# Performance work log

Measured on AMD Instinct MI355X. Metric: run time of the kernel, lower is better.

Reference implementation:

```python
import jax, jax.numpy as jnp
import numpy as np

H = 64   # LSTM hidden size
NL = 8   # LSTM layers
B, T = 2048, 64


def setup_inputs() -> dict:
    key = jax.random.key(0)
    ks = jax.random.split(key, 18)
    r = lambda i, shape, s=0.1: jax.random.normal(ks[i], shape, dtype=jnp.float32) * s
    return {
        "x": r(0, (B, T, 2), 1.0),
        "w1": r(1, (16, 2)), "b1": r(2, (16,)),
        "w2": r(3, (16, 16)), "b2": r(4, (16,)),
        "w_ih0": r(5, (4 * H, 16)), "w_hh0": r(6, (4 * H, H)),
        "b_ih0": r(7, (4 * H,)), "b_hh0": r(8, (4 * H,)),
        "w_ih": r(9, (NL - 1, 4 * H, H)), "w_hh": r(10, (NL - 1, 4 * H, H)),
        "b_ih": r(11, (NL - 1, 4 * H)), "b_hh": r(12, (NL - 1, 4 * H)),
        "wo1": r(13, (32, H)), "bo1": r(14, (32,)),
        "wo2": r(15, (4, 32)), "bo2": r(16, (4,)),
    }


def _lstm_layer(x, w_ih, w_hh, b):
    # x: [B, T, I]; torch gate order: i, f, g, o
    bsz = x.shape[0]
    xg = jnp.einsum('bti,gi->btg', x, w_ih) + b  # [B, T, 4H] precomputed input gates

    def step(carry, xg_t):
        h, c = carry
        gates = xg_t + h @ w_hh.T
        i, f, g, o = jnp.split(gates, 4, axis=-1)
        i = jax.nn.sigmoid(i); f = jax.nn.sigmoid(f)
        g = jnp.tanh(g); o = jax.nn.sigmoid(o)
        c = f * c + i * g
        h = o * jnp.tanh(c)
        return (h, c), h

    h0 = jnp.zeros((bsz, H), x.dtype)
    _, hs = jax.lax.scan(step, (h0, h0), jnp.swapaxes(xg, 0, 1))  # [T, B, H]
    return jnp.swapaxes(hs, 0, 1)


def reference(x, w1, b1, w2, b2, w_ih0, w_hh0, b_ih0, b_hh0,
              w_ih, w_hh, b_ih, b_hh, wo1, bo1, wo2, bo2):
    # action-input MLP: 2 -> 16 -> relu -> 16
    h = jax.nn.relu(x @ w1.T + b1) @ w2.T + b2
    # 8-layer LSTM, hidden 64
    h = _lstm_layer(h, w_ih0, w_hh0, b_ih0 + b_hh0)
    for l in range(NL - 1):
        h = _lstm_layer(h, w_ih[l], w_hh[l], b_ih[l] + b_hh[l])
    # output MLP: 64 -> 32 -> relu -> 4
    return jax.nn.relu(h @ wo1.T + bo1) @ wo2.T + bo2
```

## Files before the change

kernel.cpp:

```cpp
#include <hip/hip_runtime.h>


#define BATCH 2048
#define TT 64
#define HH 64
#define LDP 136

typedef short bf16x8 __attribute__((ext_vector_type(8)));
typedef float f32x4 __attribute__((ext_vector_type(4)));

__device__ __forceinline__ float sigmoid_fast(float x) {
    return __builtin_amdgcn_rcpf(1.f + __expf(-x));
}
__device__ __forceinline__ float tanh_fast(float x) {
    float e = __expf(-2.f * x);
    e = fminf(e, 1e30f);
    return (1.f - e) * __builtin_amdgcn_rcpf(1.f + e);
}
__device__ __forceinline__ void split2(float x, unsigned short& hi, unsigned short& lo) {
    const unsigned u = __float_as_uint(x);
    hi = (unsigned short)(u >> 16);
    const float r = x - __uint_as_float(u & 0xFFFF0000u);
    lo = (unsigned short)(__float_as_uint(r) >> 16);
}
__device__ __forceinline__ void wg_wait(int* c, int v) {
    while (__hip_atomic_load(c, __ATOMIC_ACQUIRE, __HIP_MEMORY_SCOPE_WORKGROUP) < v)
        __builtin_amdgcn_s_sleep(1);
}
__device__ __forceinline__ void wg_bump(int* c, int lane) {
    if (lane == 0)
        __hip_atomic_fetch_add(c, 1, __ATOMIC_RELEASE, __HIP_MEMORY_SCOPE_WORKGROUP);
}

__global__ __launch_bounds__(256)
void mlp_in_kernel(const float* __restrict__ x,
                   const float* __restrict__ w1, const float* __restrict__ b1,
                   const float* __restrict__ w2, const float* __restrict__ b2,
                   float* __restrict__ out) {
    const int gid = blockIdx.x * 256 + threadIdx.x;
    const float x0 = x[gid * 2 + 0];
    const float x1 = x[gid * 2 + 1];
    float hid[16];
#pragma unroll
    for (int j = 0; j < 16; ++j) {
        float v = fmaf(x1, w1[j * 2 + 1], fmaf(x0, w1[j * 2 + 0], b1[j]));
        hid[j] = fmaxf(0.f, v);
    }
    float o[16];
#pragma unroll
    for (int oo = 0; oo < 16; ++oo) {
        float acc = b2[oo];
#pragma unroll
        for (int j = 0; j < 16; ++j) acc = fmaf(hid[j], w2[oo * 16 + j], acc);
        o[oo] = acc;
    }
    float4* op = (float4*)(out + gid * 16);
#pragma unroll
    for (int q = 0; q < 4; ++q) {
        float4 v;
        v.x = o[q * 4 + 0]; v.y = o[q * 4 + 1]; v.z = o[q * 4 + 2]; v.w = o[q * 4 + 3];
        op[q] = v;
    }
}

template <int IA, int IPADA>
__global__ __launch_bounds__(512, 2)
void lstm_pair(const float* __restrict__ xmlp,
               unsigned* __restrict__ P,
               float* __restrict__ houtf,
               const int last,
               const float* __restrict__ wihA, const float* __restrict__ whhA,
               const float* __restrict__ biA, const float* __restrict__ bhA,
               const float* __restrict__ wihB, const float* __restrict__ whhB,
               const float* __restrict__ biB, const float* __restrict__ bhB) {
    constexpr int KTA = (IPADA + 64) / 32;
    __shared__ unsigned short pAh[2][16 * LDP], pAl[2][16 * LDP];
    __shared__ unsigned short pBh[2][16 * LDP], pBl[2][16 * LDP];
    __shared__ int cA, cB;

    const int tid = threadIdx.x;
    const int wv = tid >> 6, lane = tid & 63, l16 = lane & 15, quad = lane >> 4;
    const int grp = wv >> 2;
    const int wg = wv & 3;
    const int base = blockIdx.x * 8;
    const bool lo32 = (lane < 32);
    const int bpi = (lane & 31) << 2;

    if (tid == 0) { cA = 0; cB = 0; }
    for (int e = tid; e < 2 * 16 * LDP; e += 512) {
        (&pAh[0][0])[e] = 0; (&pAl[0][0])[e] = 0;
        (&pBh[0][0])[e] = 0; (&pBl[0][0])[e] = 0;
    }

    const int I    = grp ? 64 : IA;
    const int IPAD = grp ? 64 : IPADA;
    const int KT   = grp ? 4  : KTA;
    const float* wih = grp ? wihB : wihA;
    const float* whh = grp ? whhB : whhA;
    const float* bi  = grp ? biB  : biA;
    const float* bh  = grp ? bhB  : bhA;

    const int jg = 16 * wg + l16;
    bf16x8 bhi[4][4], blo[4][4];
    float bsum[4];
#pragma unroll
    for (int gt = 0; gt < 4; ++gt) {
        const int n = gt * 64 + jg;
        bsum[gt] = bi[n] + bh[n];
#pragma unroll
        for (int kt = 0; kt < 4; ++kt) {
            bf16x8 vh = {0, 0, 0, 0, 0, 0, 0, 0};
            bf16x8 vl = {0, 0, 0, 0, 0, 0, 0, 0};
            if (kt < KT) {
#pragma unroll
                for (int j = 0; j < 8; ++j) {
                    const int k = kt * 32 + quad * 8 + j;
                    float w = 0.f;
                    if (k < I) w = wih[n * I + k];
                    else if (k >= IPAD) w = whh[n * 64 + (k - IPAD)];
                    unsigned short h_, l_;
                    split2(w, h_, l_);
                    vh[j] = (short)h_;
                    vl[j] = (short)l_;
                }
            }
            bhi[kt][gt] = vh;
            blo[kt][gt] = vl;
        }
    }

    float cs[2] = {0.f, 0.f};
    const int row0 = (quad & 1) * 4 + ((quad >> 1) << 1);

    float xrf = 0.f;
    uint2 xru = {0u, 0u};
    int sr = 0, sc = 0;
    if (grp == 0) {
        if (IA == 16) {
            sr = tid >> 4; sc = tid & 15;
            if (tid < 128) {
                xrf = xmlp[((size_t)(base + sr) * TT + 0) * 16 + sc];
                unsigned short h_, l_;
                split2(xrf, h_, l_);
                pAh[0][sr * LDP + sc] = h_;
                pAl[0][sr * LDP + sc] = l_;
                xrf = xmlp[((size_t)(base + sr) * TT + 1) * 16 + sc];
            }
        } else {
            sr = tid >> 5; sc = (tid & 31) * 2;
            xru = *(const uint2*)&P[((size_t)(base + sr) * TT + 0) * 64 + sc];
            pAh[0][sr * LDP + sc + 0] = (unsigned short)(xru.x >> 16);
            pAl[0][sr * LDP + sc + 0] = (unsigned short)(xru.x & 0xffffu);
            pAh[0][sr * LDP + sc + 1] = (unsigned short)(xru.y >> 16);
            pAl[0][sr * LDP + sc + 1] = (unsigned short)(xru.y & 0xffffu);
            xru = *(const uint2*)&P[((size_t)(base + sr) * TT + 1) * 64 + sc];
        }
    }
    __syncthreads();

    if (grp == 0) {
        for (int t = 0; t < TT; ++t) {
            const int pb = t & 1;
            if (t) {
                wg_wait(&cA, 4 * t);
                if (t >= 2) wg_wait(&cB, 4 * (t - 1));
            }
            f32x4 a0[4], a1[4], a2[4];
#pragma unroll
            for (int gt = 0; gt < 4; ++gt) {
                a0[gt][0] = bsum[gt]; a0[gt][1] = bsum[gt];
                a0[gt][2] = bsum[gt]; a0[gt][3] = bsum[gt];
                a1[gt] = (f32x4){0.f, 0.f, 0.f, 0.f};
                a2[gt] = (f32x4){0.f, 0.f, 0.f, 0.f};
            }
#pragma unroll
            for (int kt = 0; kt < KTA; ++kt) {
                const int aoff = l16 * LDP + kt * 32 + quad * 8;
                const bf16x8 ahi = *(const bf16x8*)&pAh[pb][aoff];
                const bf16x8 alo = *(const bf16x8*)&pAl[pb][aoff];
#pragma unroll
                for (int gt = 0; gt < 4; ++gt) {
                    a0[gt] = __builtin_amdgcn_mfma_f32_16x16x32_bf16(ahi, bhi[kt][gt], a0[gt], 0, 0, 0);
                    a1[gt] = __builtin_amdgcn_mfma_f32_16x16x32_bf16(alo, bhi[kt][gt], a1[gt], 0, 0, 0);
                    a2[gt] = __builtin_amdgcn_mfma_f32_16x16x32_bf16(ahi, blo[kt][gt], a2[gt], 0, 0, 0);
                }
            }
            f32x4 s4[4];
#pragma unroll
            for (int gt = 0; gt < 4; ++gt) s4[gt] = (a0[gt] + a1[gt]) + a2[gt];
            float gk[4][2];
#pragma unroll
            for (int gt = 0; gt < 4; ++gt) {
#pragma unroll
                for (int r = 0; r < 2; ++r) {
                    const float up = __uint_as_float(
                        __builtin_amdgcn_ds_bpermute(bpi, __float_as_uint(s4[gt][r + 2])));
                    gk[gt][r] = lo32 ? s4[gt][r] : up;
                }
            }
#pragma unroll
            for (int r = 0; r < 2; ++r) {
                const float iv = sigmoid_fast(gk[0][r]);
                const float fv = sigmoid_fast(gk[1][r]);
                const float gv = tanh_fast(gk[2][r]);
                const float ov = sigmoid_fast(gk[3][r]);
                const float cn = fv * cs[r] + iv * gv;
                cs[r] = cn;
                const float h = ov * tanh_fast(cn);
                const int R = row0 + r;
                unsigned short h_, l_;
                split2(h, h_, l_);
                pAh[pb ^ 1][R * LDP + IPADA + jg] = h_;
                pAl[pb ^ 1][R * LDP + IPADA + jg] = l_;
                pBh[pb][R * LDP + jg] = h_;
                pBl[pb][R * LDP + jg] = l_;
            }
            if (IA == 16) {
                if (tid < 128) {
                    unsigned short h_, l_;
                    split2(xrf, h_, l_);
                    pAh[pb ^ 1][sr * LDP + sc] = h_;
                    pAl[pb ^ 1][sr * LDP + sc] = l_;
                    const int tp = (t + 2) & (TT - 1);
                    xrf = xmlp[((size_t)(base + sr) * TT + tp) * 16 + sc];
                }
            } else {
                pAh[pb ^ 1][sr * LDP + sc + 0] = (unsigned short)(xru.x >> 16);
                pAl[pb ^ 1][sr * LDP + sc + 0] = (unsigned short)(xru.x & 0xffffu);
                pAh[pb ^ 1][sr * LDP + sc + 1] = (unsigned short)(xru.y >> 16);
                pAl[pb ^ 1][sr * LDP + sc + 1] = (unsigned short)(xru.y & 0xffffu);
                const int tp = (t + 2) & (TT - 1);
                xru = *(const uint2*)&P[((size_t)(base + sr) * TT + tp) * 64 + sc];
            }
            wg_bump(&cA, lane);
        }
    } else {
        for (int t = 0; t < TT; ++t) {
            const int pb = t & 1;
            wg_wait(&cA, 4 * (t + 1));
            if (t) wg_wait(&cB, 4 * t);
            f32x4 a0[4], a1[4], a2[4];
#pragma unroll
            for (int gt = 0; gt < 4; ++gt) {
                a0[gt][0] = bsum[gt]; a0[gt][1] = bsum[gt];
                a0[gt][2] = bsum[gt]; a0[gt][3] = bsum[gt];
                a1[gt] = (f32x4){0.f, 0.f, 0.f, 0.f};
                a2[gt] = (f32x4){0.f, 0.f, 0.f, 0.f};
            }
#pragma unroll
            for (int kt = 0; kt < 4; ++kt) {
                const int aoff = l16 * LDP + kt * 32 + quad * 8;
                const bf16x8 ahi = *(const bf16x8*)&pBh[pb][aoff];
                const bf16x8 alo = *(const bf16x8*)&pBl[pb][aoff];
#pragma unroll
                for (int gt = 0; gt < 4; ++gt) {
                    a0[gt] = __builtin_amdgcn_mfma_f32_16x16x32_bf16(ahi, bhi[kt][gt], a0[gt], 0, 0, 0);
                    a1[gt] = __builtin_amdgcn_mfma_f32_16x16x32_bf16(alo, bhi[kt][gt], a1[gt], 0, 0, 0);
                    a2[gt] = __builtin_amdgcn_mfma_f32_16x16x32_bf16(ahi, blo[kt][gt], a2[gt], 0, 0, 0);
                }
            }
            f32x4 s4[4];
#pragma unroll
            for (int gt = 0; gt < 4; ++gt) s4[gt] = (a0[gt] + a1[gt]) + a2[gt];
            float gk[4][2];
#pragma unroll
            for (int gt = 0; gt < 4; ++gt) {
#pragma unroll
                for (int r = 0; r < 2; ++r) {
                    const float up = __uint_as_float(
                        __builtin_amdgcn_ds_bpermute(bpi, __float_as_uint(s4[gt][r + 2])));
                    gk[gt][r] = lo32 ? s4[gt][r] : up;
                }
            }
#pragma unroll
            for (int r = 0; r < 2; ++r) {
                const float iv = sigmoid_fast(gk[0][r]);
                const float fv = sigmoid_fast(gk[1][r]);
                const float gv = tanh_fast(gk[2][r]);
                const float ov = sigmoid_fast(gk[3][r]);
                const float cn = fv * cs[r] + iv * gv;
                cs[r] = cn;
                const float h = ov * tanh_fast(cn);
                const int R = row0 + r;
                unsigned short h_, l_;
                split2(h, h_, l_);
                pBh[pb ^ 1][R * LDP + 64 + jg] = h_;
                pBl[pb ^ 1][R * LDP + 64 + jg] = l_;
                if (!last) {
                    P[((size_t)(base + R) * TT + t) * 64 + jg] =
                        ((unsigned)h_ << 16) | (unsigned)l_;
                } else {
                    houtf[((size_t)(base + R) * TT + t) * HH + jg] = h;
                }
            }
            wg_bump(&cB, lane);
        }
    }
}

__global__ __launch_bounds__(256)
void mlp_out_kernel(const float* __restrict__ hin,
                    const float* __restrict__ wo1, const float* __restrict__ bo1,
                    const float* __restrict__ wo2, const float* __restrict__ bo2,
                    float* __restrict__ out) {
    __shared__ __align__(16) float wo1_s[32 * 64];
    __shared__ float bo1_s[32];
    __shared__ float wo2_s[4 * 32];
    __shared__ float bo2_s[4];
    const int tid = threadIdx.x;
    for (int e = tid; e < 32 * 64; e += 256) wo1_s[e] = wo1[e];
    if (tid < 32) bo1_s[tid] = bo1[tid];
    if (tid < 128) wo2_s[tid] = wo2[tid];
    if (tid < 4) bo2_s[tid] = bo2[tid];
    __syncthreads();

    const int gid = blockIdx.x * 256 + tid;
    const float4* hv = (const float4*)(hin + gid * 64);
    float4 h[16];
#pragma unroll
    for (int q = 0; q < 16; ++q) h[q] = hv[q];

    float m1[32];
#pragma unroll
    for (int o = 0; o < 32; ++o) {
        float acc = bo1_s[o];
        const float4* wrow = (const float4*)(wo1_s + o * 64);
#pragma unroll
        for (int q = 0; q < 16; ++q) {
            const float4 w = wrow[q];
            acc = fmaf(h[q].x, w.x, acc);
            acc = fmaf(h[q].y, w.y, acc);
            acc = fmaf(h[q].z, w.z, acc);
            acc = fmaf(h[q].w, w.w, acc);
        }
        m1[o] = fmaxf(0.f, acc);
    }
    float r[4];
#pragma unroll
    for (int q = 0; q < 4; ++q) {
        float acc = bo2_s[q];
#pragma unroll
        for (int o = 0; o < 32; ++o) acc = fmaf(m1[o], wo2_s[q * 32 + o], acc);
        r[q] = acc;
    }
    float4 res;
    res.x = r[0]; res.y = r[1]; res.z = r[2]; res.w = r[3];
    ((float4*)out)[gid] = res;
}

extern "C" void kernel_launch(void* const* d_in, const int* in_sizes, int n_in,
                              void* d_out, int out_size, void* d_ws, size_t ws_size,
                              hipStream_t stream) {
    const float* x     = (const float*)d_in[0];
    const float* w1    = (const float*)d_in[1];
    const float* b1    = (const float*)d_in[2];
    const float* w2    = (const float*)d_in[3];
    const float* b2    = (const float*)d_in[4];
    const float* w_ih0 = (const float*)d_in[5];
    const float* w_hh0 = (const float*)d_in[6];
    const float* b_ih0 = (const float*)d_in[7];
    const float* b_hh0 = (const float*)d_in[8];
    const float* w_ih  = (const float*)d_in[9];
    const float* w_hh  = (const float*)d_in[10];
    const float* b_ih  = (const float*)d_in[11];
    const float* b_hh  = (const float*)d_in[12];
    const float* wo1   = (const float*)d_in[13];
    const float* bo1   = (const float*)d_in[14];
    const float* wo2   = (const float*)d_in[15];
    const float* bo2   = (const float*)d_in[16];

    float* buf_mlp = (float*)d_ws;
    unsigned* P = (unsigned*)(buf_mlp + (size_t)BATCH * TT * 16);
    float* bufH = (float*)(P + (size_t)BATCH * TT * 64);

    const int nbt_blocks = (BATCH * TT) / 256;

    mlp_in_kernel<<<nbt_blocks, 256, 0, stream>>>(x, w1, b1, w2, b2, buf_mlp);

    lstm_pair<16, 32><<<BATCH / 8, 512, 0, stream>>>(
        buf_mlp, P, bufH, 0,
        w_ih0, w_hh0, b_ih0, b_hh0,
        w_ih + (size_t)0 * 256 * 64, w_hh + (size_t)0 * 256 * 64, b_ih + 0 * 256, b_hh + 0 * 256);

    for (int p = 1; p < 4; ++p) {
        const int la = 2 * p - 1, lb = 2 * p;
        lstm_pair<64, 64><<<BATCH / 8, 512, 0, stream>>>(
            buf_mlp, P, bufH, (p == 3) ? 1 : 0,
            w_ih + (size_t)la * 256 * 64, w_hh + (size_t)la * 256 * 64,
            b_ih + la * 256, b_hh + la * 256,
            w_ih + (size_t)lb * 256 * 64, w_hh + (size_t)lb * 256 * 64,
            b_ih + lb * 256, b_hh + lb * 256);
    }

    mlp_out_kernel<<<nbt_blocks, 256, 0, stream>>>(bufH, wo1, bo1, wo2, bo2, (float*)d_out);
}
```

Measured before the change: 511.3 us.

## Read layer-A recurrent h from shared B buffer, vectorize staging, drop spin sleep

Layer A no longer writes its hidden state twice into LDS. Its MFMA loop now reads the input-tile part from a narrower pA buffer and the recurrent part from the pB buffer that layer B already consumes. Input staging is moved to the start of each step and uses packed 32-bit LDS stores. The spin-wait drops its s_sleep, and the MFMA loops are wrapped in s_setprio to favour matrix issue. These changes cut LDS store traffic and handoff latency per timestep. The cost is busier polling and reliance on the existing double-buffer ordering to keep pB reads safe.

```diff
diff --git a/kernel.cpp b/kernel.cpp
--- a/kernel.cpp
+++ b/kernel.cpp
@@ -24,8 +24,7 @@
     lo = (unsigned short)(__float_as_uint(r) >> 16);
 }
 __device__ __forceinline__ void wg_wait(int* c, int v) {
-    while (__hip_atomic_load(c, __ATOMIC_ACQUIRE, __HIP_MEMORY_SCOPE_WORKGROUP) < v)
-        __builtin_amdgcn_s_sleep(1);
+    while (__hip_atomic_load(c, __ATOMIC_ACQUIRE, __HIP_MEMORY_SCOPE_WORKGROUP) < v) {}
 }
 __device__ __forceinline__ void wg_bump(int* c, int lane) {
     if (lane == 0)
@@ -74,8 +73,10 @@
                const float* __restrict__ wihB, const float* __restrict__ whhB,
                const float* __restrict__ biB, const float* __restrict__ bhB) {
     constexpr int KTA = (IPADA + 64) / 32;
-    __shared__ unsigned short pAh[2][16 * LDP], pAl[2][16 * LDP];
-    __shared__ unsigned short pBh[2][16 * LDP], pBl[2][16 * LDP];
+    constexpr int KTX = IPADA / 32;
+    constexpr int LDPA = IPADA + 8;
+    __shared__ __align__(16) unsigned short pAh[2][16 * LDPA], pAl[2][16 * LDPA];
+    __shared__ __align__(16) unsigned short pBh[2][16 * LDP], pBl[2][16 * LDP];
     __shared__ int cA, cB;
 
     const int tid = threadIdx.x;
@@ -87,10 +88,8 @@
     const int bpi = (lane & 31) << 2;
 
     if (tid == 0) { cA = 0; cB = 0; }
-    for (int e = tid; e < 2 * 16 * LDP; e += 512) {
-        (&pAh[0][0])[e] = 0; (&pAl[0][0])[e] = 0;
-        (&pBh[0][0])[e] = 0; (&pBl[0][0])[e] = 0;
-    }
+    for (int e = tid; e < 2 * 16 * LDPA; e += 512) { (&pAh[0][0])[e] = 0; (&pAl[0][0])[e] = 0; }
+    for (int e = tid; e < 2 * 16 * LDP; e += 512)  { (&pBh[0][0])[e] = 0; (&pBl[0][0])[e] = 0; }
 
     const int I    = grp ? 64 : IA;
     const int IPAD = grp ? 64 : IPADA;
@@ -132,27 +131,28 @@
     float cs[2] = {0.f, 0.f};
     const int row0 = (quad & 1) * 4 + ((quad >> 1) << 1);
 
-    float xrf = 0.f;
+    float2 xr2 = {0.f, 0.f};
     uint2 xru = {0u, 0u};
     int sr = 0, sc = 0;
+    bool stg = false;
     if (grp == 0) {
         if (IA == 16) {
-            sr = tid >> 4; sc = tid & 15;
-            if (tid < 128) {
-                xrf = xmlp[((size_t)(base + sr) * TT + 0) * 16 + sc];
-                unsigned short h_, l_;
-                split2(xrf, h_, l_);
-                pAh[0][sr * LDP + sc] = h_;
-                pAl[0][sr * LDP + sc] = l_;
-                xrf = xmlp[((size_t)(base + sr) * TT + 1) * 16 + sc];
+            stg = (tid < 128);
+            sr = tid >> 3; sc = (tid & 7) * 2;
+            if (stg) {
+                xr2 = *(const float2*)&xmlp[((size_t)(base + sr) * TT + 0) * 16 + sc];
+                unsigned short h0, l0, h1, l1;
+                split2(xr2.x, h0, l0); split2(xr2.y, h1, l1);
+                *(unsigned*)&pAh[0][sr * LDPA + sc] = ((unsigned)h1 << 16) | h0;
+                *(unsigned*)&pAl[0][sr * LDPA + sc] = ((unsigned)l1 << 16) | l0;
+                xr2 = *(const float2*)&xmlp[((size_t)(base + sr) * TT + 1) * 16 + sc];
             }
         } else {
+            stg = true;
             sr = tid >> 5; sc = (tid & 31) * 2;
             xru = *(const uint2*)&P[((size_t)(base + sr) * TT + 0) * 64 + sc];
-            pAh[0][sr * LDP + sc + 0] = (unsigned short)(xru.x >> 16);
-            pAl[0][sr * LDP + sc + 0] = (unsigned short)(xru.x & 0xffffu);
-            pAh[0][sr * LDP + sc + 1] = (unsigned short)(xru.y >> 16);
-            pAl[0][sr * LDP + sc + 1] = (unsigned short)(xru.y & 0xffffu);
+            *(unsigned*)&pAh[0][sr * LDPA + sc] = (xru.y & 0xFFFF0000u) | (xru.x >> 16);
+            *(unsigned*)&pAl[0][sr * LDPA + sc] = (xru.y << 16) | (xru.x & 0xFFFFu);
             xru = *(const uint2*)&P[((size_t)(base + sr) * TT + 1) * 64 + sc];
         }
     }
@@ -165,6 +165,21 @@
                 wg_wait(&cA, 4 * t);
                 if (t >= 2) wg_wait(&cB, 4 * (t - 1));
             }
+            if (stg) {
+                if (IA == 16) {
+                    unsigned short h0, l0, h1, l1;
+                    split2(xr2.x, h0, l0); split2(xr2.y, h1, l1);
+                    *(unsigned*)&pAh[pb ^ 1][sr * LDPA + sc] = ((unsigned)h1 << 16) | h0;
+                    *(unsigned*)&pAl[pb ^ 1][sr * LDPA + sc] = ((unsigned)l1 << 16) | l0;
+                    const int tp = (t + 2) & (TT - 1);
+                    xr2 = *(const float2*)&xmlp[((size_t)(base + sr) * TT + tp) * 16 + sc];
+                } else {
+                    *(unsigned*)&pAh[pb ^ 1][sr * LDPA + sc] = (xru.y & 0xFFFF0000u) | (xru.x >> 16);
+                    *(unsigned*)&pAl[pb ^ 1][sr * LDPA + sc] = (xru.y << 16) | (xru.x & 0xFFFFu);
+                    const int tp = (t + 2) & (TT - 1);
+                    xru = *(const uint2*)&P[((size_t)(base + sr) * TT + tp) * 64 + sc];
+                }
+            }
             f32x4 a0[4], a1[4], a2[4];
 #pragma unroll
             for (int gt = 0; gt < 4; ++gt) {
@@ -173,11 +188,19 @@
                 a1[gt] = (f32x4){0.f, 0.f, 0.f, 0.f};
                 a2[gt] = (f32x4){0.f, 0.f, 0.f, 0.f};
             }
+            __builtin_amdgcn_s_setprio(1);
 #pragma unroll
             for (int kt = 0; kt < KTA; ++kt) {
-                const int aoff = l16 * LDP + kt * 32 + quad * 8;
-                const bf16x8 ahi = *(const bf16x8*)&pAh[pb][aoff];
-                const bf16x8 alo = *(const bf16x8*)&pAl[pb][aoff];
+                bf16x8 ahi, alo;
+                if (kt < KTX) {
+                    const int aoff = l16 * LDPA + kt * 32 + quad * 8;
+                    ahi = *(const bf16x8*)&pAh[pb][aoff];
+                    alo = *(const bf16x8*)&pAl[pb][aoff];
+                } else {
+                    const int aoff = l16 * LDP + (kt - KTX) * 32 + quad * 8;
+                    ahi = *(const bf16x8*)&pBh[pb ^ 1][aoff];
+                    alo = *(const bf16x8*)&pBl[pb ^ 1][aoff];
+                }
 #pragma unroll
                 for (int gt = 0; gt < 4; ++gt) {
                     a0[gt] = __builtin_amdgcn_mfma_f32_16x16x32_bf16(ahi, bhi[kt][gt], a0[gt], 0, 0, 0);
@@ -185,6 +208,7 @@
                     a2[gt] = __builtin_amdgcn_mfma_f32_16x16x32_bf16(ahi, blo[kt][gt], a2[gt], 0, 0, 0);
                 }
             }
+            __builtin_amdgcn_s_setprio(0);
             f32x4 s4[4];
 #pragma unroll
             for (int gt = 0; gt < 4; ++gt) s4[gt] = (a0[gt] + a1[gt]) + a2[gt];
@@ -210,27 +234,8 @@
                 const int R = row0 + r;
                 unsigned short h_, l_;
                 split2(h, h_, l_);
-                pAh[pb ^ 1][R * LDP + IPADA + jg] = h_;
-                pAl[pb ^ 1][R * LDP + IPADA + jg] = l_;
                 pBh[pb][R * LDP + jg] = h_;
                 pBl[pb][R * LDP + jg] = l_;
-            }
-            if (IA == 16) {
-                if (tid < 128) {
-                    unsigned short h_, l_;
-                    split2(xrf, h_, l_);
-                    pAh[pb ^ 1][sr * LDP + sc] = h_;
-                    pAl[pb ^ 1][sr * LDP + sc] = l_;
-                    const int tp = (t + 2) & (TT - 1);
-                    xrf = xmlp[((size_t)(base + sr) * TT + tp) * 16 + sc];
-                }
-            } else {
-                pAh[pb ^ 1][sr * LDP + sc + 0] = (unsigned short)(xru.x >> 16);
-                pAl[pb ^ 1][sr * LDP + sc + 0] = (unsigned short)(xru.x & 0xffffu);
-                pAh[pb ^ 1][sr * LDP + sc + 1] = (unsigned short)(xru.y >> 16);
-                pAl[pb ^ 1][sr * LDP + sc + 1] = (unsigned short)(xru.y & 0xffffu);
-                const int tp = (t + 2) & (TT - 1);
-                xru = *(const uint2*)&P[((size_t)(base + sr) * TT + tp) * 64 + sc];
             }
             wg_bump(&cA, lane);
         }
@@ -247,6 +252,7 @@
                 a1[gt] = (f32x4){0.f, 0.f, 0.f, 0.f};
                 a2[gt] = (f32x4){0.f, 0.f, 0.f, 0.f};
             }
+            __builtin_amdgcn_s_setprio(1);
 #pragma unroll
             for (int kt = 0; kt < 4; ++kt) {
                 const int aoff = l16 * LDP + kt * 32 + quad * 8;
@@ -259,6 +265,7 @@
                     a2[gt] = __builtin_amdgcn_mfma_f32_16x16x32_bf16(ahi, blo[kt][gt], a2[gt], 0, 0, 0);
                 }
             }
+            __builtin_amdgcn_s_setprio(0);
             f32x4 s4[4];
 #pragma unroll
             for (int gt = 0; gt < 4; ++gt) s4[gt] = (a0[gt] + a1[gt]) + a2[gt];
```

Result: no change. 518.1 us (+1.3%).
